# Kernel optimization log

Hardware: AMD Instinct MI355X
Metric: run time of the kernel (lower is better)

The kernel has to match this reference:

```python
import jax, jax.numpy as jnp
import numpy as np

EPS = 1e-5

def _bn(x, g, b, m, v):
    # inference-mode BatchNorm2d over NCHW
    inv = g / jnp.sqrt(v + EPS)
    return x * inv[None, :, None, None] + (b - m * inv)[None, :, None, None]

def _adder2d(x, w, stride, pad):
    # AdderNet 'convolution': out = -sum_{c,kh,kw} |patch - w|
    B, C, H, W = x.shape
    O, _, k, _ = w.shape
    xp = jnp.pad(x, ((0, 0), (0, 0), (pad, pad), (pad, pad)))
    Ho = (H + 2 * pad - k) // stride + 1
    Wo = (W + 2 * pad - k) // stride + 1
    # unfold: [B, C, k*k, Ho, Wo] with (C, kh, kw) ordering matching w.reshape
    cols = jnp.stack([xp[:, :, i:i + stride * Ho:stride, j:j + stride * Wo:stride]
                      for i in range(k) for j in range(k)], axis=2)
    cols = cols.reshape(B, C * k * k, Ho * Wo)            # [B, CKK, L]
    wf = w.reshape(O, C * k * k)                          # [O, CKK]
    out = -jnp.sum(jnp.abs(cols[:, None, :, :] - wf[None, :, :, None]), axis=2)  # [B,O,L]
    return out.reshape(B, O, Ho, Wo)

def setup_inputs() -> dict:
    key = jax.random.key(0)
    ks = jax.random.split(key, 16)
    C = 64
    return {
        "x": jax.random.normal(ks[0], (4, C, 32, 32), jnp.float32),
        "bn1_g": jax.random.uniform(ks[1], (C,), jnp.float32),
        "bn1_b": jax.random.normal(ks[2], (C,), jnp.float32),
        "bn1_m": jax.random.normal(ks[3], (C,), jnp.float32),
        "bn1_v": jax.random.uniform(ks[4], (C,), jnp.float32),
        "w1": jax.random.normal(ks[5], (C, C, 3, 3), jnp.float32),
        "bn2_g": jax.random.uniform(ks[6], (C,), jnp.float32),
        "bn2_b": jax.random.normal(ks[7], (C,), jnp.float32),
        "bn2_m": jax.random.normal(ks[8], (C,), jnp.float32),
        "bn2_v": jax.random.uniform(ks[9], (C,), jnp.float32),
        "w2": jax.random.normal(ks[10], (C, C, 3, 3), jnp.float32),
        "fc1_w": jax.random.normal(ks[11], (C // 16, C), jnp.float32) * 0.1,
        "fc1_b": jax.random.normal(ks[12], (C // 16,), jnp.float32) * 0.1,
        "fc2_w": jax.random.normal(ks[13], (C, C // 16), jnp.float32) * 0.1,
        "fc2_b": jax.random.normal(ks[14], (C,), jnp.float32) * 0.1,
    }

def reference(x, bn1_g, bn1_b, bn1_m, bn1_v, w1,
              bn2_g, bn2_b, bn2_m, bn2_v, w2,
              fc1_w, fc1_b, fc2_w, fc2_b):
    out = jax.nn.relu(_bn(x, bn1_g, bn1_b, bn1_m, bn1_v))
    shortcut = x  # stride==1 and in_planes==planes -> identity shortcut
    out = _adder2d(out, w1, 1, 1)
    out = _adder2d(jax.nn.relu(_bn(out, bn2_g, bn2_b, bn2_m, bn2_v)), w2, 1, 1)
    # SE gate: global avg pool -> fc1 -> relu -> fc2 -> sigmoid
    s = out.mean(axis=(2, 3))                              # [B, planes]
    h = jax.nn.relu(s @ fc1_w.T + fc1_b)
    g = jax.nn.sigmoid(h @ fc2_w.T + fc2_b)
    return out * g[:, :, None, None] + shortcut
```

## Files before the change

kernel.cpp:

```cpp
#include <hip/hip_runtime.h>
#include <math.h>

#define NELEM   262144
#define PIMG    1296
#define PPADN   165888
#define NHALO   16896
#define EPS_BN  1e-5f
#define QSC     128.0f
#define QBIAS_F 16384.5f
#define QZ_W    0x40004000u
#define QINV    (1.0f / 128.0f)

__device__ __forceinline__ unsigned sad16(unsigned a, unsigned b, unsigned acc) {
    asm("v_sad_u16 %0, %1, %2, %0" : "+v"(acc) : "v"(a), "v"(b));
    return acc;
}
__device__ __forceinline__ unsigned qu(float v) {
    return (unsigned)(int)fmaf(v, QSC, QBIAS_F);
}

__global__ __launch_bounds__(256, 4) void adder1_kernel(
    const float* __restrict__ x,
    const float* __restrict__ g1, const float* __restrict__ b1,
    const float* __restrict__ m1, const float* __restrict__ v1,
    const float* __restrict__ w1,
    const float* __restrict__ g2, const float* __restrict__ b2,
    const float* __restrict__ m2, const float* __restrict__ v2,
    unsigned* __restrict__ qout, float* __restrict__ sbuf)
{
    __shared__ unsigned smem[7680];
    unsigned (*xs)[6][36]    = reinterpret_cast<unsigned(*)[6][36]>(smem);
    unsigned (*red)[32][9]   = reinterpret_cast<unsigned(*)[32][9]>(smem);
    unsigned (*wlds)[32][12] = reinterpret_cast<unsigned(*)[32][12]>(smem + 6912);

    const int blk = blockIdx.x;
    const int sp  = blk & 7;
    const int og  = (blk >> 3) & 31;
    const int b   = blk >> 8;
    const int t   = threadIdx.x;

    const int gid = blk * 256 + t;
    if (gid < 256) sbuf[gid] = 0.f;
    if (gid < NHALO) {
        int img = gid / 132;
        int j   = gid - img * 132;
        int r, c;
        if (j < 34)       { r = 0;          c = j;       }
        else if (j < 68)  { r = 33;         c = j - 34;  }
        else if (j < 100) { r = j - 68 + 1; c = 0;       }
        else              { r = j - 100 + 1; c = 33;     }
        qout[img * PIMG + r * 36 + c] = QZ_W;
    }

    for (int i = t; i < 576; i += 256) {
        int o_i = i / 288;
        int rem = i - o_i * 288;
        int pr  = rem / 9;
        int kk  = rem - pr * 9;
        int woff = ((og * 2 + o_i) * 64 + pr * 2) * 9 + kk;
        wlds[o_i][pr][kk] = qu(w1[woff]) | (qu(w1[woff + 9]) << 16);
    }

    for (int u = t; u < 192; u += 256) {
        const int pair = u / 6;
        const int lr   = u - pair * 6;
        const int xrow = sp * 4 + lr - 1;
        unsigned* dst  = &xs[pair][lr][0];
        if (xrow < 0 || xrow > 31) {
#pragma unroll
            for (int k = 0; k < 9; ++k)
                reinterpret_cast<uint4*>(dst)[k] = make_uint4(QZ_W, QZ_W, QZ_W, QZ_W);
        } else {
            const int c0 = pair * 2;
            const float inv0 = g1[c0]     * rsqrtf(v1[c0]     + EPS_BN);
            const float bet0 = b1[c0]     - m1[c0]     * inv0;
            const float inv1 = g1[c0 + 1] * rsqrtf(v1[c0 + 1] + EPS_BN);
            const float bet1 = b1[c0 + 1] - m1[c0 + 1] * inv1;
            const float* x0p = x + ((b * 64 + c0) * 32 + xrow) * 32;
            const float* x1p = x0p + 1024;
#pragma unroll
            for (int k = 0; k < 9; ++k) {
                unsigned q[4];
#pragma unroll
                for (int e = 0; e < 4; ++e) {
                    int c = k * 4 + e;
                    unsigned qv = QZ_W;
                    if (c >= 1 && c <= 32) {
                        float a0 = fmaxf(fmaf(x0p[c - 1], inv0, bet0), 0.f);
                        float a1 = fmaxf(fmaf(x1p[c - 1], inv1, bet1), 0.f);
                        qv = qu(a0) | (qu(a1) << 16);
                    }
                    q[e] = qv;
                }
                reinterpret_cast<uint4*>(dst)[k] = make_uint4(q[0], q[1], q[2], q[3]);
            }
        }
    }
    __syncthreads();

    const int pos = t & 31;
    const int cq  = t >> 5;
    const int y_i = pos >> 3;
    const int x0  = (pos & 7) * 4;

    unsigned acc[2][4];
#pragma unroll
    for (int oo = 0; oo < 2; ++oo)
#pragma unroll
        for (int xi = 0; xi < 4; ++xi) acc[oo][xi] = 0u;

#pragma unroll
    for (int j = 0; j < 4; ++j) {
        const int pr = cq * 4 + j;
        unsigned p[3][6];
#pragma unroll
        for (int r = 0; r < 3; ++r) {
            const unsigned* src = &xs[pr][y_i + r][x0];
            uint4 a0 = *reinterpret_cast<const uint4*>(src);
            uint2 a1 = *reinterpret_cast<const uint2*>(src + 4);
            p[r][0] = a0.x; p[r][1] = a0.y; p[r][2] = a0.z; p[r][3] = a0.w;
            p[r][4] = a1.x; p[r][5] = a1.y;
        }
#pragma unroll
        for (int oo = 0; oo < 2; ++oo) {
            uint4 wa = *reinterpret_cast<const uint4*>(&wlds[oo][pr][0]);
            uint4 wb = *reinterpret_cast<const uint4*>(&wlds[oo][pr][4]);
            unsigned w8 = wlds[oo][pr][8];
            unsigned wv[9] = {wa.x, wa.y, wa.z, wa.w,
                              wb.x, wb.y, wb.z, wb.w, w8};
#pragma unroll
            for (int kh = 0; kh < 3; ++kh)
#pragma unroll
                for (int kw = 0; kw < 3; ++kw) {
                    unsigned ww = wv[kh * 3 + kw];
#pragma unroll
                    for (int xi = 0; xi < 4; ++xi)
                        acc[oo][xi] = sad16(p[kh][xi + kw], ww, acc[oo][xi]);
                }
        }
    }
    __syncthreads();

    {
        unsigned* dst = &red[cq][pos][0];
#pragma unroll
        for (int z = 0; z < 8; ++z) dst[z] = acc[z >> 2][z & 3];
    }
    __syncthreads();

    const int oo2 = t >> 7;
    const int yy2 = (t >> 5) & 3;
    const int xx2 = t & 31;
    const int pp  = yy2 * 8 + (xx2 >> 2);
    const int z   = oo2 * 4 + (xx2 & 3);
    unsigned total = 0;
#pragma unroll
    for (int q = 0; q < 8; ++q) total += red[q][pp][z];

    const int o  = og * 2 + oo2;
    const int gy = sp * 4 + yy2;

    float inv = g2[o] * rsqrtf(v2[o] + EPS_BN);
    float cc0 = -inv * QINV;
    float cc1 = b2[o] - m2[o] * inv;
    float a2  = fmaxf(fmaf((float)total, cc0, cc1), 0.f);
    unsigned short qv = (unsigned short)(int)fmaf(a2, QSC, QBIAS_F);
    size_t widx = (size_t)(b * 32 + (o >> 1)) * PIMG + (gy + 1) * 36 + (xx2 + 1);
    reinterpret_cast<unsigned short*>(qout)[widx * 2 + (o & 1)] = qv;
}

__global__ __launch_bounds__(256, 4) void adder2_kernel(
    const unsigned* __restrict__ qsrc, const float* __restrict__ w2,
    float* __restrict__ fout, float* __restrict__ sbuf)
{
    __shared__ unsigned wlds[2][32][12];
    __shared__ unsigned red[8][32][9];

    const int blk = blockIdx.x;
    const int sp  = blk & 7;
    const int og  = (blk >> 3) & 31;
    const int b   = blk >> 8;
    const int t   = threadIdx.x;
    const int pos = t & 31;
    const int cq  = t >> 5;
    const int y_i = pos >> 3;
    const int x0  = (pos & 7) * 4;

    for (int i = t; i < 576; i += 256) {
        int o_i = i / 288;
        int rem = i - o_i * 288;
        int pr  = rem / 9;
        int kk  = rem - pr * 9;
        int woff = ((og * 2 + o_i) * 64 + pr * 2) * 9 + kk;
        wlds[o_i][pr][kk] = qu(w2[woff]) | (qu(w2[woff + 9]) << 16);
    }
    __syncthreads();

    unsigned acc[2][4];
#pragma unroll
    for (int oo = 0; oo < 2; ++oo)
#pragma unroll
        for (int xi = 0; xi < 4; ++xi) acc[oo][xi] = 0u;

#pragma unroll
    for (int j = 0; j < 4; ++j) {
        const int pr = cq * 4 + j;
        const unsigned* pc = qsrc + (size_t)(b * 32 + pr) * PIMG
                                  + (sp * 4 + y_i) * 36 + x0;
        unsigned p[3][6];
#pragma unroll
        for (int r = 0; r < 3; ++r) {
            uint4 a0 = *reinterpret_cast<const uint4*>(pc + r * 36);
            uint2 a1 = *reinterpret_cast<const uint2*>(pc + r * 36 + 4);
            p[r][0] = a0.x; p[r][1] = a0.y; p[r][2] = a0.z; p[r][3] = a0.w;
            p[r][4] = a1.x; p[r][5] = a1.y;
        }
#pragma unroll
        for (int oo = 0; oo < 2; ++oo) {
            uint4 wa = *reinterpret_cast<const uint4*>(&wlds[oo][pr][0]);
            uint4 wb = *reinterpret_cast<const uint4*>(&wlds[oo][pr][4]);
            unsigned w8 = wlds[oo][pr][8];
            unsigned wv[9] = {wa.x, wa.y, wa.z, wa.w,
                              wb.x, wb.y, wb.z, wb.w, w8};
#pragma unroll
            for (int kh = 0; kh < 3; ++kh)
#pragma unroll
                for (int kw = 0; kw < 3; ++kw) {
                    unsigned ww = wv[kh * 3 + kw];
#pragma unroll
                    for (int xi = 0; xi < 4; ++xi)
                        acc[oo][xi] = sad16(p[kh][xi + kw], ww, acc[oo][xi]);
                }
        }
    }

    {
        unsigned* dst = &red[cq][pos][0];
#pragma unroll
        for (int z = 0; z < 8; ++z) dst[z] = acc[z >> 2][z & 3];
    }
    __syncthreads();

    const int oo2 = t >> 7;
    const int yy2 = (t >> 5) & 3;
    const int xx2 = t & 31;
    const int pp  = yy2 * 8 + (xx2 >> 2);
    const int z   = oo2 * 4 + (xx2 & 3);
    unsigned total = 0;
#pragma unroll
    for (int q = 0; q < 8; ++q) total += red[q][pp][z];

    const int o  = og * 2 + oo2;
    const int gy = sp * 4 + yy2;

    float v = -(float)total * QINV;
    fout[((b * 64 + o) * 32 + gy) * 32 + xx2] = v;
    float sum = v;
#pragma unroll
    for (int off = 32; off > 0; off >>= 1)
        sum += __shfl_down(sum, off, 64);
    if ((t & 63) == 0) atomicAdd(&sbuf[b * 64 + o], sum);
}

__global__ __launch_bounds__(256) void gate_kernel(
    const float* __restrict__ out2, const float* __restrict__ x,
    const float* __restrict__ sbuf,
    const float* __restrict__ fc1w, const float* __restrict__ fc1b,
    const float* __restrict__ fc2w, const float* __restrict__ fc2b,
    float* __restrict__ out)
{
    const int bo = blockIdx.x;
    const int b  = bo >> 6;
    const int o  = bo & 63;
    const int t  = threadIdx.x;

    __shared__ float ss[64];
    if (t < 64) ss[t] = sbuf[b * 64 + t] * (1.f / 1024.f);
    __syncthreads();

    float h[4];
#pragma unroll
    for (int j = 0; j < 4; ++j) {
        float a = fc1b[j];
#pragma unroll
        for (int c = 0; c < 64; ++c) a += ss[c] * fc1w[j * 64 + c];
        h[j] = fmaxf(a, 0.f);
    }
    float zz = fc2b[o];
#pragma unroll
    for (int j = 0; j < 4; ++j) zz += h[j] * fc2w[o * 4 + j];
    float g = 1.f / (1.f + __expf(-zz));

    const int base = bo * 1024 + t * 4;
    float4 v  = *reinterpret_cast<const float4*>(out2 + base);
    float4 xv = *reinterpret_cast<const float4*>(x + base);
    float4 r;
    r.x = v.x * g + xv.x;
    r.y = v.y * g + xv.y;
    r.z = v.z * g + xv.z;
    r.w = v.w * g + xv.w;
    *reinterpret_cast<float4*>(out + base) = r;
}

extern "C" void kernel_launch(void* const* d_in, const int* in_sizes, int n_in,
                              void* d_out, int out_size, void* d_ws, size_t ws_size,
                              hipStream_t stream)
{
    const float* x    = (const float*)d_in[0];
    const float* bn1g = (const float*)d_in[1];
    const float* bn1b = (const float*)d_in[2];
    const float* bn1m = (const float*)d_in[3];
    const float* bn1v = (const float*)d_in[4];
    const float* w1   = (const float*)d_in[5];
    const float* bn2g = (const float*)d_in[6];
    const float* bn2b = (const float*)d_in[7];
    const float* bn2m = (const float*)d_in[8];
    const float* bn2v = (const float*)d_in[9];
    const float* w2   = (const float*)d_in[10];
    const float* fc1w = (const float*)d_in[11];
    const float* fc1b = (const float*)d_in[12];
    const float* fc2w = (const float*)d_in[13];
    const float* fc2b = (const float*)d_in[14];

    unsigned* ws     = (unsigned*)d_ws;
    unsigned* qout1p = ws;
    float*    out2   = (float*)(ws + PPADN);
    float*    sbuf   = (float*)(ws + PPADN + NELEM);

    adder1_kernel<<<1024, 256, 0, stream>>>(x, bn1g, bn1b, bn1m, bn1v, w1,
                                            bn2g, bn2b, bn2m, bn2v,
                                            qout1p, sbuf);
    adder2_kernel<<<1024, 256, 0, stream>>>(qout1p, w2, out2, sbuf);
    gate_kernel<<<256, 256, 0, stream>>>(out2, x, sbuf, fc1w, fc1b, fc2w, fc2b,
                                         (float*)d_out);
}
```

Baseline: 114.7 us.

## Fuse SE gate into adder2 via last-block counter and coalesce adder1 staging

Removes the separate gate kernel launch. Each batch image gets an atomic ticket counter, and the last adder2 block to finish for that image computes the SE MLP and applies the gated residual over the whole image. Adder1's input and weight staging is also rewritten: BN coefficients are precomputed in shared memory, the tile is prefilled with the zero code, and the loads are coalesced element-wise with 16-bit scattered writes. The trade-off is that the final elementwise pass now runs on only 4 blocks (one per image) instead of 256, which serialises 64K elements per block.

```diff
diff --git a/kernel.cpp b/kernel.cpp
--- a/kernel.cpp
+++ b/kernel.cpp
@@ -26,12 +26,15 @@
     const float* __restrict__ w1,
     const float* __restrict__ g2, const float* __restrict__ b2,
     const float* __restrict__ m2, const float* __restrict__ v2,
-    unsigned* __restrict__ qout, float* __restrict__ sbuf)
+    unsigned* __restrict__ qout, float* __restrict__ sbuf,
+    unsigned* __restrict__ cnt)
 {
-    __shared__ unsigned smem[7680];
+    __shared__ unsigned smem[7808];
     unsigned (*xs)[6][36]    = reinterpret_cast<unsigned(*)[6][36]>(smem);
     unsigned (*red)[32][9]   = reinterpret_cast<unsigned(*)[32][9]>(smem);
     unsigned (*wlds)[32][12] = reinterpret_cast<unsigned(*)[32][12]>(smem + 6912);
+    float* binv = reinterpret_cast<float*>(smem + 7680);
+    float* bbet = binv + 64;
 
     const int blk = blockIdx.x;
     const int sp  = blk & 7;
@@ -41,58 +44,53 @@
 
     const int gid = blk * 256 + t;
     if (gid < 256) sbuf[gid] = 0.f;
+    else if (gid < 272) cnt[gid - 256] = 0u;
     if (gid < NHALO) {
         int img = gid / 132;
         int j   = gid - img * 132;
         int r, c;
-        if (j < 34)       { r = 0;          c = j;       }
-        else if (j < 68)  { r = 33;         c = j - 34;  }
-        else if (j < 100) { r = j - 68 + 1; c = 0;       }
-        else              { r = j - 100 + 1; c = 33;     }
+        if (j < 34)       { r = 0;           c = j;       }
+        else if (j < 68)  { r = 33;          c = j - 34;  }
+        else if (j < 100) { r = j - 68 + 1;  c = 0;       }
+        else              { r = j - 100 + 1; c = 33;      }
         qout[img * PIMG + r * 36 + c] = QZ_W;
     }
 
-    for (int i = t; i < 576; i += 256) {
-        int o_i = i / 288;
-        int rem = i - o_i * 288;
-        int pr  = rem / 9;
-        int kk  = rem - pr * 9;
-        int woff = ((og * 2 + o_i) * 64 + pr * 2) * 9 + kk;
-        wlds[o_i][pr][kk] = qu(w1[woff]) | (qu(w1[woff + 9]) << 16);
-    }
-
-    for (int u = t; u < 192; u += 256) {
-        const int pair = u / 6;
-        const int lr   = u - pair * 6;
-        const int xrow = sp * 4 + lr - 1;
-        unsigned* dst  = &xs[pair][lr][0];
-        if (xrow < 0 || xrow > 31) {
-#pragma unroll
-            for (int k = 0; k < 9; ++k)
-                reinterpret_cast<uint4*>(dst)[k] = make_uint4(QZ_W, QZ_W, QZ_W, QZ_W);
-        } else {
-            const int c0 = pair * 2;
-            const float inv0 = g1[c0]     * rsqrtf(v1[c0]     + EPS_BN);
-            const float bet0 = b1[c0]     - m1[c0]     * inv0;
-            const float inv1 = g1[c0 + 1] * rsqrtf(v1[c0 + 1] + EPS_BN);
-            const float bet1 = b1[c0 + 1] - m1[c0 + 1] * inv1;
-            const float* x0p = x + ((b * 64 + c0) * 32 + xrow) * 32;
-            const float* x1p = x0p + 1024;
-#pragma unroll
-            for (int k = 0; k < 9; ++k) {
-                unsigned q[4];
-#pragma unroll
-                for (int e = 0; e < 4; ++e) {
-                    int c = k * 4 + e;
-                    unsigned qv = QZ_W;
-                    if (c >= 1 && c <= 32) {
-                        float a0 = fmaxf(fmaf(x0p[c - 1], inv0, bet0), 0.f);
-                        float a1 = fmaxf(fmaf(x1p[c - 1], inv1, bet1), 0.f);
-                        qv = qu(a0) | (qu(a1) << 16);
-                    }
-                    q[e] = qv;
-                }
-                reinterpret_cast<uint4*>(dst)[k] = make_uint4(q[0], q[1], q[2], q[3]);
+    if (t < 64) {
+        float iv = g1[t] * rsqrtf(v1[t] + EPS_BN);
+        binv[t] = iv;
+        bbet[t] = b1[t] - m1[t] * iv;
+    }
+
+    for (int u = t; u < 1728; u += 256)
+        reinterpret_cast<uint4*>(smem)[u] = make_uint4(QZ_W, QZ_W, QZ_W, QZ_W);
+
+    {
+        unsigned short* wh = reinterpret_cast<unsigned short*>(wlds);
+        const float* wbase = w1 + og * 1152;
+        for (int u = t; u < 1152; u += 256) {
+            int o_i = u / 576;
+            int rem = u - o_i * 576;
+            int c   = rem / 9;
+            int kk  = rem - c * 9;
+            wh[((o_i * 32 + (c >> 1)) * 12 + kk) * 2 + (c & 1)] =
+                (unsigned short)qu(wbase[u]);
+        }
+    }
+    __syncthreads();
+
+    {
+        unsigned short* xh = reinterpret_cast<unsigned short*>(smem);
+        for (int u = t; u < 12288; u += 256) {
+            int lr  = u >> 11;
+            int c   = (u >> 5) & 63;
+            int col = u & 31;
+            int xrow = sp * 4 + lr - 1;
+            if ((unsigned)xrow < 32u) {
+                float xv = x[(b * 64 + c) * 1024 + xrow * 32 + col];
+                unsigned q = qu(fmaxf(fmaf(xv, binv[c], bbet[c]), 0.f));
+                xh[((c >> 1) * 216 + lr * 36 + col + 1) * 2 + (c & 1)] =
+                    (unsigned short)q;
             }
         }
     }
@@ -171,10 +169,17 @@
 
 __global__ __launch_bounds__(256, 4) void adder2_kernel(
     const unsigned* __restrict__ qsrc, const float* __restrict__ w2,
-    float* __restrict__ fout, float* __restrict__ sbuf)
+    const float* __restrict__ x,
+    const float* __restrict__ fc1w, const float* __restrict__ fc1b,
+    const float* __restrict__ fc2w, const float* __restrict__ fc2b,
+    float* __restrict__ fout, float* __restrict__ sbuf,
+    unsigned* __restrict__ cnt, float* __restrict__ out)
 {
     __shared__ unsigned wlds[2][32][12];
     __shared__ unsigned red[8][32][9];
+    __shared__ float gg[64];
+    __shared__ float hh[4];
+    __shared__ int lastflag;
 
     const int blk = blockIdx.x;
     const int sp  = blk & 7;
@@ -260,46 +265,51 @@
     for (int off = 32; off > 0; off >>= 1)
         sum += __shfl_down(sum, off, 64);
     if ((t & 63) == 0) atomicAdd(&sbuf[b * 64 + o], sum);
-}
-
-__global__ __launch_bounds__(256) void gate_kernel(
-    const float* __restrict__ out2, const float* __restrict__ x,
-    const float* __restrict__ sbuf,
-    const float* __restrict__ fc1w, const float* __restrict__ fc1b,
-    const float* __restrict__ fc2w, const float* __restrict__ fc2b,
-    float* __restrict__ out)
-{
-    const int bo = blockIdx.x;
-    const int b  = bo >> 6;
-    const int o  = bo & 63;
-    const int t  = threadIdx.x;
-
-    __shared__ float ss[64];
-    if (t < 64) ss[t] = sbuf[b * 64 + t] * (1.f / 1024.f);
-    __syncthreads();
-
-    float h[4];
-#pragma unroll
-    for (int j = 0; j < 4; ++j) {
-        float a = fc1b[j];
-#pragma unroll
-        for (int c = 0; c < 64; ++c) a += ss[c] * fc1w[j * 64 + c];
-        h[j] = fmaxf(a, 0.f);
-    }
-    float zz = fc2b[o];
-#pragma unroll
-    for (int j = 0; j < 4; ++j) zz += h[j] * fc2w[o * 4 + j];
-    float g = 1.f / (1.f + __expf(-zz));
-
-    const int base = bo * 1024 + t * 4;
-    float4 v  = *reinterpret_cast<const float4*>(out2 + base);
-    float4 xv = *reinterpret_cast<const float4*>(x + base);
-    float4 r;
-    r.x = v.x * g + xv.x;
-    r.y = v.y * g + xv.y;
-    r.z = v.z * g + xv.z;
-    r.w = v.w * g + xv.w;
-    *reinterpret_cast<float4*>(out + base) = r;
+
+    __syncthreads();
+    if (t == 0) {
+        __threadfence();
+        unsigned tk = __hip_atomic_fetch_add(&cnt[b], 1u, __ATOMIC_ACQ_REL,
+                                             __HIP_MEMORY_SCOPE_AGENT);
+        lastflag = (tk == 255u);
+        if (lastflag) __threadfence();
+    }
+    __syncthreads();
+    if (!lastflag) return;
+
+    if (t < 64) gg[t] = sbuf[b * 64 + t] * (1.f / 1024.f);
+    __syncthreads();
+    if (t < 4) {
+        float a = fc1b[t];
+#pragma unroll
+        for (int c = 0; c < 64; ++c) a += gg[c] * fc1w[t * 64 + c];
+        hh[t] = fmaxf(a, 0.f);
+    }
+    __syncthreads();
+    if (t < 64) {
+        float zz = fc2b[t];
+#pragma unroll
+        for (int j = 0; j < 4; ++j) zz += hh[j] * fc2w[t * 4 + j];
+        gg[t] = 1.f / (1.f + __expf(-zz));
+    }
+    __syncthreads();
+
+    const float* o2b = fout + b * 65536;
+    const float* xb  = x    + b * 65536;
+    float*       ob  = out  + b * 65536;
+#pragma unroll 8
+    for (int i = 0; i < 64; ++i) {
+        float g = gg[i];
+        int idx = i * 1024 + t * 4;
+        float4 vv = *reinterpret_cast<const float4*>(o2b + idx);
+        float4 xv = *reinterpret_cast<const float4*>(xb + idx);
+        float4 r;
+        r.x = vv.x * g + xv.x;
+        r.y = vv.y * g + xv.y;
+        r.z = vv.z * g + xv.z;
+        r.w = vv.w * g + xv.w;
+        *reinterpret_cast<float4*>(ob + idx) = r;
+    }
 }
 
 extern "C" void kernel_launch(void* const* d_in, const int* in_sizes, int n_in,
@@ -323,14 +333,15 @@
     const float* fc2b = (const float*)d_in[14];
 
     unsigned* ws     = (unsigned*)d_ws;
-    unsigned* qout1p = ws;
-    float*    out2   = (float*)(ws + PPADN);
-    float*    sbuf   = (float*)(ws + PPADN + NELEM);
+    float*    sbuf   = (float*)ws;
+    unsigned* cnt    = ws + 256;
+    unsigned* qout1p = ws + 512;
+    float*    out2   = (float*)(ws + 512 + PPADN);
 
     adder1_kernel<<<1024, 256, 0, stream>>>(x, bn1g, bn1b, bn1m, bn1v, w1,
                                             bn2g, bn2b, bn2m, bn2v,
-                                            qout1p, sbuf);
-    adder2_kernel<<<1024, 256, 0, stream>>>(qout1p, w2, out2, sbuf);
-    gate_kernel<<<256, 256, 0, stream>>>(out2, x, sbuf, fc1w, fc1b, fc2w, fc2b,
-                                         (float*)d_out);
-}
+                                            qout1p, sbuf, cnt);
+    adder2_kernel<<<1024, 256, 0, stream>>>(qout1p, w2, x,
+                                            fc1w, fc1b, fc2w, fc2b,
+                                            out2, sbuf, cnt, (float*)d_out);
+}
```

Result: slower. 198.5 us (+73.0%).
